# Optimization experiments

Measured on AMD Instinct MI355X. Metric: run time of the kernel, lower is better.

The kernel has to match this reference:

```python
import jax, jax.numpy as jnp
import numpy as np

B, S = 8, 2048  # batch, seq_len; D == S required by matmul(value, qk)


def setup_inputs() -> dict:
    key = jax.random.key(0)
    kq, kk, kv = jax.random.split(key, 3)
    return {
        "query": jax.random.normal(kq, (B, S, S), dtype=jnp.float32),
        "key": jax.random.normal(kk, (B, S, S), dtype=jnp.float32),
        "value": jax.random.normal(kv, (B, S, S), dtype=jnp.float32),
        "attn_mask": jnp.zeros((S, S), dtype=jnp.float32),
    }


def reference(query, key, value, attn_mask):
    # qk = query @ key^T  -> [B, S, S]
    qk = jnp.einsum("bqd,bkd->bqk", query, key)
    # dropout with p=0.0 is the identity
    # softmax over the last dim (torch .softmax() intended dim=-1)
    qk = jax.nn.softmax(qk, axis=-1)
    # matmul(value, qk): [B, S, S] @ [B, S, S] -> [B, S, S]
    out = jnp.einsum("bsd,bdk->bsk", value, qk)
    return out
```

## Files before the change

### kernel.cpp

```cpp
#include <hip/hip_runtime.h>
#include <hip/hip_fp16.h>

typedef _Float16 f16;
typedef _Float16 f16x8 __attribute__((ext_vector_type(8)));
typedef _Float16 f16x4 __attribute__((ext_vector_type(4)));
typedef float f32x4 __attribute__((ext_vector_type(4)));
typedef float f32x16 __attribute__((ext_vector_type(16)));

#define SEQ 2048
#define BATCH 8
#define NCHUNK 16

__device__ __forceinline__ void gl2lds16(const f16* g, f16* l) {
  __builtin_amdgcn_global_load_lds((const __attribute__((address_space(1))) void*)g,
                                   (__attribute__((address_space(3))) void*)l,
                                   16, 0, 0);
}

__global__ __launch_bounds__(256) void cast_kernel(const float* __restrict__ in,
                                                   f16* __restrict__ out, int n4) {
  int i = blockIdx.x * 256 + threadIdx.x;
  if (i < n4) {
    float4 v = ((const float4*)in)[i];
    f16x4 h;
    h[0] = (f16)v.x; h[1] = (f16)v.y; h[2] = (f16)v.z; h[3] = (f16)v.w;
    ((f16x4*)out)[i] = h;
  }
}

__global__ __launch_bounds__(256) void gemm_nt(const f16* __restrict__ A,
                                               const f16* __restrict__ Bt,
                                               float* __restrict__ C,
                                               int K, int N,
                                               long long sA, long long sB, long long sC) {
  const f16* Ab = A + blockIdx.z * sA;
  const f16* Bb = Bt + blockIdx.z * sB;
  float* Cb = C + blockIdx.z * sC;
  const int m0 = blockIdx.y * 128, n0 = blockIdx.x * 128;

  __shared__ f16 As[128][32];
  __shared__ f16 Bs[128][32];

  const int tid = threadIdx.x;
  const int wave = tid >> 6, lane = tid & 63;
  const int wm = (wave >> 1) << 6;
  const int wn = (wave & 1) << 6;
  const int l31 = lane & 31, h = lane >> 5;

  const int lrow = lane >> 2;
  const int lcol = (lane & 3) * 8;

  f32x16 acc[2][2];
#pragma unroll
  for (int i = 0; i < 2; i++)
#pragma unroll
    for (int j = 0; j < 2; j++)
#pragma unroll
      for (int r = 0; r < 16; r++) acc[i][j][r] = 0.f;

  for (int k0 = 0; k0 < K; k0 += 32) {
#pragma unroll
    for (int i = 0; i < 2; i++) {
      const int rb = (i * 4 + wave) * 16;
      gl2lds16(Ab + (size_t)(m0 + rb + lrow) * K + k0 + lcol, &As[rb][0]);
      gl2lds16(Bb + (size_t)(n0 + rb + lrow) * K + k0 + lcol, &Bs[rb][0]);
    }
    __syncthreads();

#pragma unroll
    for (int s = 0; s < 2; s++) {
      f16x8 a0 = *(const f16x8*)&As[wm + l31][s * 16 + h * 8];
      f16x8 a1 = *(const f16x8*)&As[wm + 32 + l31][s * 16 + h * 8];
      f16x8 b0 = *(const f16x8*)&Bs[wn + l31][s * 16 + h * 8];
      f16x8 b1 = *(const f16x8*)&Bs[wn + 32 + l31][s * 16 + h * 8];
      acc[0][0] = __builtin_amdgcn_mfma_f32_32x32x16_f16(a0, b0, acc[0][0], 0, 0, 0);
      acc[0][1] = __builtin_amdgcn_mfma_f32_32x32x16_f16(a0, b1, acc[0][1], 0, 0, 0);
      acc[1][0] = __builtin_amdgcn_mfma_f32_32x32x16_f16(a1, b0, acc[1][0], 0, 0, 0);
      acc[1][1] = __builtin_amdgcn_mfma_f32_32x32x16_f16(a1, b1, acc[1][1], 0, 0, 0);
    }
    __syncthreads();
  }

#pragma unroll
  for (int i = 0; i < 2; i++) {
#pragma unroll
    for (int j = 0; j < 2; j++) {
      const int colb = n0 + wn + j * 32 + l31;
      const int rowb = m0 + wm + i * 32 + 4 * h;
#pragma unroll
      for (int r = 0; r < 16; r++) {
        const int row = rowb + (r & 3) + 8 * (r >> 2);
        Cb[(size_t)row * N + colb] = acc[i][j][r];
      }
    }
  }
}

__global__ __launch_bounds__(256) void colstats_part(const float* __restrict__ G,
                                                     float* __restrict__ pm,
                                                     float* __restrict__ ps) {
  const int b = blockIdx.z, chunk = blockIdx.y;
  const int q = blockIdx.x * 256 + threadIdx.x;
  const int rows = SEQ / NCHUNK;
  const float* p = G + (size_t)b * SEQ * SEQ + (size_t)chunk * rows * SEQ + q;
  float m = -3.0e38f, s = 0.f;
#pragma unroll 4
  for (int k = 0; k < rows; k++) {
    float x = p[(size_t)k * SEQ];
    if (x > m) { s = s * __expf(m - x) + 1.f; m = x; }
    else       { s += __expf(x - m); }
  }
  const size_t o = ((size_t)chunk * BATCH + b) * SEQ + q;
  pm[o] = m;
  ps[o] = s;
}

__global__ __launch_bounds__(256) void colstats_combine(const float* __restrict__ pm,
                                                        const float* __restrict__ ps,
                                                        float* __restrict__ mrow,
                                                        float* __restrict__ rzrow) {
  const int b = blockIdx.y;
  const int q = blockIdx.x * 256 + threadIdx.x;
  float m = -3.0e38f, s = 0.f;
#pragma unroll
  for (int c = 0; c < NCHUNK; c++) {
    const size_t o = ((size_t)c * BATCH + b) * SEQ + q;
    float mc = pm[o], sc = ps[o];
    if (mc > m) { s = s * __expf(m - mc) + sc; m = mc; }
    else        { s += sc * __expf(mc - m); }
  }
  mrow[(size_t)b * SEQ + q] = m;
  rzrow[(size_t)b * SEQ + q] = 1.f / s;
}

__global__ __launch_bounds__(256) void scale_kernel(const float* __restrict__ G,
                                                    const float* __restrict__ mrow,
                                                    const float* __restrict__ rzrow,
                                                    f16* __restrict__ PT) {
  const int i = blockIdx.x * 256 + threadIdx.x;
  const int b = i >> 20;
  const int cg = i & (SEQ / 4 - 1);
  float4 g = ((const float4*)G)[i];
  float4 m4 = ((const float4*)(mrow + (size_t)b * SEQ))[cg];
  float4 z4 = ((const float4*)(rzrow + (size_t)b * SEQ))[cg];
  f16x4 o;
  o[0] = (f16)(__expf(g.x - m4.x) * z4.x);
  o[1] = (f16)(__expf(g.y - m4.y) * z4.y);
  o[2] = (f16)(__expf(g.z - m4.z) * z4.z);
  o[3] = (f16)(__expf(g.w - m4.w) * z4.w);
  ((f16x4*)PT)[i] = o;
}

extern "C" void kernel_launch(void* const* d_in, const int* in_sizes, int n_in,
                              void* d_out, int out_size, void* d_ws, size_t ws_size,
                              hipStream_t stream) {
  const float* Q = (const float*)d_in[0];
  const float* Kf = (const float*)d_in[1];
  const float* V = (const float*)d_in[2];
  float* out = (float*)d_out;

  const size_t nElem = (size_t)BATCH * SEQ * SEQ;
  f16* Qh = (f16*)d_ws;
  f16* Kh = Qh + nElem;
  f16* Vh = Kh + nElem;
  f16* PT = Vh + nElem;
  float* G = (float*)(PT + nElem);
  float* mrow = G + nElem;
  float* rzrow = mrow + (size_t)BATCH * SEQ;
  float* pm = (float*)Qh;
  float* ps = pm + (size_t)NCHUNK * BATCH * SEQ;

  const int n4 = (int)(nElem / 4);
  dim3 cgrid(n4 / 256);
  cast_kernel<<<cgrid, 256, 0, stream>>>(Q, Qh, n4);
  cast_kernel<<<cgrid, 256, 0, stream>>>(Kf, Kh, n4);
  cast_kernel<<<cgrid, 256, 0, stream>>>(V, Vh, n4);

  const long long sb = (long long)SEQ * SEQ;
  dim3 ggrid(SEQ / 128, SEQ / 128, BATCH);
  gemm_nt<<<ggrid, 256, 0, stream>>>(Kh, Qh, G, SEQ, SEQ, sb, sb, sb);

  colstats_part<<<dim3(SEQ / 256, NCHUNK, BATCH), 256, 0, stream>>>(G, pm, ps);
  colstats_combine<<<dim3(SEQ / 256, BATCH), 256, 0, stream>>>(pm, ps, mrow, rzrow);

  scale_kernel<<<dim3(n4 / 256), 256, 0, stream>>>(G, mrow, rzrow, PT);

  gemm_nt<<<ggrid, 256, 0, stream>>>(Vh, PT, out, SEQ, SEQ, sb, sb, sb);
}
```

Baseline: 875.8 us.

## Switch GEMM to 16x16x32 MFMA with K=64 tiles and XOR-swizzled LDS

The GEMM kernel now stages 64-wide K tiles in LDS instead of 32, halving the number of barrier pairs per K sweep. It uses an XOR swizzle on the LDS column offset to avoid bank conflicts on the f16x8 reads. It also replaces the 2x2 grid of 32x32x16 MFMAs with a 4x4 grid of 16x16x32 MFMAs per wave. This raises LDS use per block and changes the register footprint and output write pattern.

Result: slower. 902.1 us (+3.0%).

```diff
diff --git a/kernel.cpp b/kernel.cpp
--- a/kernel.cpp
+++ b/kernel.cpp
@@ -5,7 +5,6 @@
 typedef _Float16 f16x8 __attribute__((ext_vector_type(8)));
 typedef _Float16 f16x4 __attribute__((ext_vector_type(4)));
 typedef float f32x4 __attribute__((ext_vector_type(4)));
-typedef float f32x16 __attribute__((ext_vector_type(16)));
 
 #define SEQ 2048
 #define BATCH 8
@@ -38,60 +37,66 @@
   float* Cb = C + blockIdx.z * sC;
   const int m0 = blockIdx.y * 128, n0 = blockIdx.x * 128;
 
-  __shared__ f16 As[128][32];
-  __shared__ f16 Bs[128][32];
+  __shared__ f16 As[128][64];
+  __shared__ f16 Bs[128][64];
 
   const int tid = threadIdx.x;
   const int wave = tid >> 6, lane = tid & 63;
   const int wm = (wave >> 1) << 6;
   const int wn = (wave & 1) << 6;
-  const int l31 = lane & 31, h = lane >> 5;
+  const int l15 = lane & 15, h = lane >> 4;
 
-  const int lrow = lane >> 2;
-  const int lcol = (lane & 3) * 8;
+  const int srow = lane >> 3;
+  const int scol = ((lane & 7) ^ srow) * 8;
+  const f16* aSrc = Ab + (size_t)(m0 + wave * 8 + srow) * K + scol;
+  const f16* bSrc = Bb + (size_t)(n0 + wave * 8 + srow) * K + scol;
 
-  f32x16 acc[2][2];
+  const int roff = (h * 16) ^ ((l15 & 7) << 4);
+
+  f32x4 acc[4][4];
 #pragma unroll
-  for (int i = 0; i < 2; i++)
+  for (int i = 0; i < 4; i++)
 #pragma unroll
-    for (int j = 0; j < 2; j++)
+    for (int j = 0; j < 4; j++)
 #pragma unroll
-      for (int r = 0; r < 16; r++) acc[i][j][r] = 0.f;
+      for (int r = 0; r < 4; r++) acc[i][j][r] = 0.f;
 
-  for (int k0 = 0; k0 < K; k0 += 32) {
+  for (int k0 = 0; k0 < K; k0 += 64) {
 #pragma unroll
-    for (int i = 0; i < 2; i++) {
-      const int rb = (i * 4 + wave) * 16;
-      gl2lds16(Ab + (size_t)(m0 + rb + lrow) * K + k0 + lcol, &As[rb][0]);
-      gl2lds16(Bb + (size_t)(n0 + rb + lrow) * K + k0 + lcol, &Bs[rb][0]);
+    for (int j = 0; j < 4; j++) {
+      const int rb = (j * 4 + wave) * 8;
+      gl2lds16(aSrc + (size_t)(j * 32) * K + k0, &As[rb][0]);
+      gl2lds16(bSrc + (size_t)(j * 32) * K + k0, &Bs[rb][0]);
     }
     __syncthreads();
 
 #pragma unroll
-    for (int s = 0; s < 2; s++) {
-      f16x8 a0 = *(const f16x8*)&As[wm + l31][s * 16 + h * 8];
-      f16x8 a1 = *(const f16x8*)&As[wm + 32 + l31][s * 16 + h * 8];
-      f16x8 b0 = *(const f16x8*)&Bs[wn + l31][s * 16 + h * 8];
-      f16x8 b1 = *(const f16x8*)&Bs[wn + 32 + l31][s * 16 + h * 8];
-      acc[0][0] = __builtin_amdgcn_mfma_f32_32x32x16_f16(a0, b0, acc[0][0], 0, 0, 0);
-      acc[0][1] = __builtin_amdgcn_mfma_f32_32x32x16_f16(a0, b1, acc[0][1], 0, 0, 0);
-      acc[1][0] = __builtin_amdgcn_mfma_f32_32x32x16_f16(a1, b0, acc[1][0], 0, 0, 0);
-      acc[1][1] = __builtin_amdgcn_mfma_f32_32x32x16_f16(a1, b1, acc[1][1], 0, 0, 0);
+    for (int kk = 0; kk < 2; kk++) {
+      const int xo = roff ^ (kk << 6);
+      f16x8 a[4], b[4];
+#pragma unroll
+      for (int i = 0; i < 4; i++) {
+        a[i] = *(const f16x8*)((const char*)(&As[0][0]) + (wm + i * 16 + l15) * 128 + xo);
+        b[i] = *(const f16x8*)((const char*)(&Bs[0][0]) + (wn + i * 16 + l15) * 128 + xo);
+      }
+#pragma unroll
+      for (int i = 0; i < 4; i++)
+#pragma unroll
+        for (int j = 0; j < 4; j++)
+          acc[i][j] = __builtin_amdgcn_mfma_f32_16x16x32_f16(a[i], b[j], acc[i][j], 0, 0, 0);
     }
     __syncthreads();
   }
 
 #pragma unroll
-  for (int i = 0; i < 2; i++) {
+  for (int i = 0; i < 4; i++) {
+    const int rowb = m0 + wm + i * 16 + h * 4;
 #pragma unroll
-    for (int j = 0; j < 2; j++) {
-      const int colb = n0 + wn + j * 32 + l31;
-      const int rowb = m0 + wm + i * 32 + 4 * h;
+    for (int j = 0; j < 4; j++) {
+      const int col = n0 + wn + j * 16 + l15;
 #pragma unroll
-      for (int r = 0; r < 16; r++) {
-        const int row = rowb + (r & 3) + 8 * (r >> 2);
-        Cb[(size_t)row * N + colb] = acc[i][j][r];
-      }
+      for (int r = 0; r < 4; r++)
+        Cb[(size_t)(rowb + r) * N + col] = acc[i][j][r];
     }
   }
 }
```
